# Kernel tuning notes

Hardware: AMD Instinct MI355X
Metric: run time of the kernel (lower is better)

The kernel has to match this reference:

```python
import jax, jax.numpy as jnp
import numpy as np

HIDDEN = 128
HEADS = 8
HEAD_DIM = HIDDEN // HEADS
N_NODES = 100000
N_EDGES = 1600000


def setup_inputs() -> dict:
    key = jax.random.key(0)
    ks = jax.random.split(key, 12)
    s = 1.0 / np.sqrt(HIDDEN)
    inp = {
        "x": jax.random.normal(ks[0], (N_NODES, HIDDEN), dtype=jnp.float32),
        "edge_index": jax.random.randint(ks[1], (2, N_EDGES), 0, N_NODES, dtype=jnp.int32),
        "edge_emb": jax.random.normal(ks[2], (N_EDGES, HIDDEN), dtype=jnp.float32),
        "q_w": jax.random.uniform(ks[3], (HIDDEN, HIDDEN), jnp.float32, -s, s),
        "q_b": jax.random.uniform(ks[4], (HIDDEN,), jnp.float32, -s, s),
        "k_w": jax.random.uniform(ks[5], (HIDDEN, HIDDEN), jnp.float32, -s, s),
        "k_b": jax.random.uniform(ks[6], (HIDDEN,), jnp.float32, -s, s),
        "v_w": jax.random.uniform(ks[7], (HIDDEN, HIDDEN), jnp.float32, -s, s),
        "v_b": jax.random.uniform(ks[8], (HIDDEN,), jnp.float32, -s, s),
        "out_w": jax.random.uniform(ks[9], (HIDDEN, HIDDEN), jnp.float32, -s, s),
        "out_b": jax.random.uniform(ks[10], (HIDDEN,), jnp.float32, -s, s),
        "eb_w": jax.random.uniform(ks[11], (HEADS, HIDDEN), jnp.float32, -s, s),
        "eb_b": jnp.zeros((HEADS,), dtype=jnp.float32),
    }
    return inp


def reference(x, edge_index, edge_emb, q_w, q_b, k_w, k_b, v_w, v_b, out_w, out_b, eb_w, eb_b):
    n = x.shape[0]
    # node projections -> [N, H, D]
    q = (x @ q_w.T + q_b).reshape(n, HEADS, HEAD_DIM)
    k = (x @ k_w.T + k_b).reshape(n, HEADS, HEAD_DIM)
    v = (x @ v_w.T + v_b).reshape(n, HEADS, HEAD_DIM)

    row, col = edge_index[0], edge_index[1]
    # per-edge scores: [E, H]
    scores = jnp.einsum('ehd,ehd->eh', q[row], k[col]) / jnp.sqrt(jnp.float32(HEAD_DIM))
    scores = scores + edge_emb @ eb_w.T + eb_b

    # segmented softmax over incoming edges of each destination node `row`
    seg_max = jax.ops.segment_max(scores, row, num_segments=n)  # [N, H]
    exp_scores = jnp.exp(scores - seg_max[row])
    seg_sum = jax.ops.segment_sum(exp_scores, row, num_segments=n)  # [N, H]
    attn = exp_scores / (seg_sum[row] + 1e-10)  # [E, H]

    # weighted scatter-aggregation of values
    weighted_v = attn[..., None] * v[col]  # [E, H, D]
    out = jax.ops.segment_sum(weighted_v, row, num_segments=n)  # [N, H, D]
    out = out.reshape(n, HIDDEN)
    return out @ out_w.T + out_b
```

## Files before the change

kernel.cpp:

```cpp
#include <hip/hip_runtime.h>

#define HID 128
#define NH 8

typedef __attribute__((ext_vector_type(8))) short short8;
typedef __attribute__((ext_vector_type(4))) float f32x4;

__device__ __forceinline__ unsigned short f2bf(float f) {
    unsigned int u = __float_as_uint(f);
    u = (u + 0x7FFF + ((u >> 16) & 1)) >> 16;
    return (unsigned short)u;
}
__device__ __forceinline__ float bf2f(unsigned short s) {
    return __uint_as_float((unsigned int)s << 16);
}
__device__ __forceinline__ unsigned int pack2bf(float lo, float hi) {
    return (unsigned int)f2bf(lo) | ((unsigned int)f2bf(hi) << 16);
}

__global__ void k_hist(const int* __restrict__ row, int E, int* __restrict__ count) {
    int i = blockIdx.x * blockDim.x + threadIdx.x;
    int stride = gridDim.x * blockDim.x;
    for (; i < E; i += stride) atomicAdd(&count[row[i]], 1);
}

__global__ void k_scan1(const int* __restrict__ in, int total,
                        int* __restrict__ out, int* __restrict__ bsums) {
    __shared__ int sd[256];
    int t = threadIdx.x;
    int base = blockIdx.x * 1024 + t * 4;
    int v0 = (base + 0 < total) ? in[base + 0] : 0;
    int v1 = (base + 1 < total) ? in[base + 1] : 0;
    int v2 = (base + 2 < total) ? in[base + 2] : 0;
    int v3 = (base + 3 < total) ? in[base + 3] : 0;
    int s = v0 + v1 + v2 + v3;
    sd[t] = s; __syncthreads();
    for (int off = 1; off < 256; off <<= 1) {
        int xx = (t >= off) ? sd[t - off] : 0;
        __syncthreads();
        sd[t] += xx;
        __syncthreads();
    }
    int excl = sd[t] - s;
    if (t == 255) bsums[blockIdx.x] = sd[255];
    int run = excl;
    if (base + 0 < total) out[base + 0] = run; run += v0;
    if (base + 1 < total) out[base + 1] = run; run += v1;
    if (base + 2 < total) out[base + 2] = run; run += v2;
    if (base + 3 < total) out[base + 3] = run;
}

__global__ void k_scan2(int* __restrict__ bs, int nb) {
    __shared__ int sd[128];
    int t = threadIdx.x;
    int vv = (t < nb) ? bs[t] : 0;
    sd[t] = vv; __syncthreads();
    for (int off = 1; off < 128; off <<= 1) {
        int xx = (t >= off) ? sd[t - off] : 0;
        __syncthreads();
        sd[t] += xx;
        __syncthreads();
    }
    if (t < nb) bs[t] = sd[t] - vv;
}

__global__ void k_scan3(int* __restrict__ out, int total, const int* __restrict__ bs) {
    int add = bs[blockIdx.x];
    int base = blockIdx.x * 1024 + threadIdx.x * 4;
    #pragma unroll
    for (int i = 0; i < 4; ++i)
        if (base + i < total) out[base + i] += add;
}

__global__ void k_cvtw(const float* __restrict__ qw, const float* __restrict__ kw,
                       const float* __restrict__ vw, const float* __restrict__ ow,
                       unsigned short* __restrict__ wbf) {
    int i = blockIdx.x * 256 + threadIdx.x;
    int idx = i * 4;
    int m = idx >> 14;
    int off = idx & 16383;
    const float* src = (m == 0) ? qw : (m == 1) ? kw : (m == 2) ? vw : ow;
    float4 v = *(const float4*)(src + off);
    ushort4 o;
    o.x = f2bf(v.x); o.y = f2bf(v.y); o.z = f2bf(v.z); o.w = f2bf(v.w);
    *(ushort4*)(wbf + idx) = o;
}

__global__ __launch_bounds__(256) void k_fat(
    const float* __restrict__ x, const unsigned short* __restrict__ wbf,
    const float* __restrict__ qb_, const float* __restrict__ kb_, const float* __restrict__ vb_,
    unsigned short* __restrict__ qkvbf, int n, int qblocks,
    const int* __restrict__ row, const int* __restrict__ col,
    const float* __restrict__ emb, const float* __restrict__ ebw,
    const float* __restrict__ ebb, const int* __restrict__ start,
    int* __restrict__ cursor, char* __restrict__ recs, int E)
{
    __shared__ __align__(16) char sm[17408];
    int bid = blockIdx.x;
    int t = threadIdx.x;

    if (bid < qblocks) {
        unsigned short (*xs)[136] = (unsigned short (*)[136])sm;
        int m0 = bid * 64;
        #pragma unroll
        for (int p = 0; p < 2; ++p) {
            int f = p * 256 + t;
            int r = f >> 3;
            int c16 = (f & 7) * 16;
            int node = m0 + r;
            float4 u0 = {0,0,0,0}, u1 = {0,0,0,0}, u2 = {0,0,0,0}, u3 = {0,0,0,0};
            if (node < n) {
                const float4* px = (const float4*)(x + (size_t)node * HID + c16);
                u0 = px[0]; u1 = px[1]; u2 = px[2]; u3 = px[3];
            }
            union { unsigned short u[8]; short8 v; } a, b;
            a.u[0]=f2bf(u0.x); a.u[1]=f2bf(u0.y); a.u[2]=f2bf(u0.z); a.u[3]=f2bf(u0.w);
            a.u[4]=f2bf(u1.x); a.u[5]=f2bf(u1.y); a.u[6]=f2bf(u1.z); a.u[7]=f2bf(u1.w);
            b.u[0]=f2bf(u2.x); b.u[1]=f2bf(u2.y); b.u[2]=f2bf(u2.z); b.u[3]=f2bf(u2.w);
            b.u[4]=f2bf(u3.x); b.u[5]=f2bf(u3.y); b.u[6]=f2bf(u3.z); b.u[7]=f2bf(u3.w);
            *(short8*)&xs[r][c16]     = a.v;
            *(short8*)&xs[r][c16 + 8] = b.v;
        }
        __syncthreads();

        int w = t >> 6, l = t & 63;
        int lr = l & 15, lc = l >> 4;
        short8 afr[4];
        #pragma unroll
        for (int c = 0; c < 4; ++c)
            afr[c] = *(const short8*)&xs[w * 16 + lr][c * 32 + lc * 8];

        #pragma unroll
        for (int m = 0; m < 3; ++m) {
            const float* bias = (m == 0) ? qb_ : (m == 1) ? kb_ : vb_;
            #pragma unroll
            for (int ct = 0; ct < 8; ++ct) {
                int colg = ct * 16 + lr;
                f32x4 acc = {0.f, 0.f, 0.f, 0.f};
                const unsigned short* wrow = wbf + (size_t)m * 16384 + (size_t)colg * 128 + lc * 8;
                #pragma unroll
                for (int c = 0; c < 4; ++c) {
                    short8 bfr = *(const short8*)(wrow + c * 32);
                    acc = __builtin_amdgcn_mfma_f32_16x16x32_bf16(afr[c], bfr, acc, 0, 0, 0);
                }
                float bv = bias[colg];
                #pragma unroll
                for (int r = 0; r < 4; ++r) {
                    int node = m0 + w * 16 + lc * 4 + r;
                    if (node < n)
                        qkvbf[(size_t)node * 384 + m * 128 + colg] = f2bf(acc[r] + bv);
                }
            }
        }
    } else {
        float (*Wx)[4][8][4] = (float (*)[4][8][4])sm;
        for (int i = t; i < 1024; i += 256) {
            int j = i & 3, g = (i >> 2) & 7, c = (i >> 5) & 3, h = i >> 7;
            Wx[h][c][g][j] = ebw[h * 128 + g * 16 + c * 4 + j];
        }
        float bbr[8];
        #pragma unroll
        for (int i = 0; i < 8; ++i) bbr[i] = ebb[i];
        __syncthreads();

        int l = t & 63;
        int g = l & 7;
        int sub = l >> 3;
        int e = (bid - qblocks) * 32 + (t >> 6) * 8 + sub;
        bool act = e < E;

        float p[8] = {0.f,0.f,0.f,0.f,0.f,0.f,0.f,0.f};
        if (act) {
            const float4* pe = (const float4*)(emb + (size_t)e * HID + g * 16);
            #pragma unroll
            for (int c = 0; c < 4; ++c) {
                float4 ev = pe[c];
                #pragma unroll
                for (int h = 0; h < 8; ++h) {
                    float4 wv = *(const float4*)&Wx[h][c][g][0];
                    p[h] += ev.x*wv.x + ev.y*wv.y + ev.z*wv.z + ev.w*wv.w;
                }
            }
        }
        #pragma unroll
        for (int off = 1; off < 8; off <<= 1) {
            #pragma unroll
            for (int h = 0; h < 8; ++h) p[h] += __shfl_xor(p[h], off);
        }
        if (act && g == 0) {
            int r = row[e];
            int ps = start[r] + atomicAdd(&cursor[r], 1);
            char* rp = recs + (size_t)ps * 32;
            uint4 r0;
            r0.x = (unsigned int)col[e];
            r0.y = pack2bf(p[0] + bbr[0], p[1] + bbr[1]);
            r0.z = pack2bf(p[2] + bbr[2], p[3] + bbr[3]);
            r0.w = pack2bf(p[4] + bbr[4], p[5] + bbr[5]);
            uint2 r1;
            r1.x = pack2bf(p[6] + bbr[6], p[7] + bbr[7]);
            r1.y = 0;
            *(uint4*)rp = r0;
            *(uint2*)(rp + 16) = r1;
        }
    }
}

__global__ __launch_bounds__(256) void k_attn(
    const unsigned short* __restrict__ qkvbf, const char* __restrict__ recs,
    const int* __restrict__ start, unsigned short* __restrict__ aout, int n)
{
    int node = blockIdx.x * 4 + (threadIdx.x >> 6);
    if (node >= n) return;
    int l = threadIdx.x & 63;
    int slot = l >> 3;
    int h = l & 7;
    int s0 = start[node];
    int deg = start[node + 1] - s0;

    float qf[16];
    {
        const unsigned short* qp = qkvbf + (size_t)node * 384 + h * 16;
        short8 q0 = *(const short8*)qp;
        short8 q1 = *(const short8*)(qp + 8);
        #pragma unroll
        for (int i = 0; i < 8; ++i) {
            qf[i] = bf2f((unsigned short)q0[i]);
            qf[8 + i] = bf2f((unsigned short)q1[i]);
        }
    }

    float acc[16];
    #pragma unroll
    for (int i = 0; i < 16; ++i) acc[i] = 0.f;
    float denom = 0.f;

    for (int base = 0; base < deg; base += 8) {
        int idx = base + slot;
        bool act = idx < deg;
        const char* rp = recs + (size_t)(s0 + (act ? idx : 0)) * 32;
        int c = act ? *(const int*)rp : 0;
        float eb = act ? bf2f(*(const unsigned short*)(rp + 4 + 2 * h)) : 0.f;
        const unsigned short* kv = qkvbf + (size_t)c * 384 + 128 + h * 16;
        short8 ka  = *(const short8*)kv;
        short8 kbv = *(const short8*)(kv + 8);
        short8 va  = *(const short8*)(kv + 128);
        short8 vb  = *(const short8*)(kv + 136);
        float part = 0.f;
        #pragma unroll
        for (int i = 0; i < 8; ++i) part += qf[i] * bf2f((unsigned short)ka[i]);
        #pragma unroll
        for (int i = 0; i < 8; ++i) part += qf[8 + i] * bf2f((unsigned short)kbv[i]);
        float es = act ? __expf(part * 0.25f + eb) : 0.f;
        denom += es;
        #pragma unroll
        for (int i = 0; i < 8; ++i) acc[i]     += es * bf2f((unsigned short)va[i]);
        #pragma unroll
        for (int i = 0; i < 8; ++i) acc[8 + i] += es * bf2f((unsigned short)vb[i]);
    }

    #pragma unroll
    for (int off = 8; off < 64; off <<= 1) {
        denom += __shfl_xor(denom, off);
        #pragma unroll
        for (int i = 0; i < 16; ++i) acc[i] += __shfl_xor(acc[i], off);
    }
    if (slot == 0) {
        float inv = 1.f / (denom + 1e-10f);
        uint4 o0, o1;
        o0.x = pack2bf(acc[0]*inv,  acc[1]*inv);
        o0.y = pack2bf(acc[2]*inv,  acc[3]*inv);
        o0.z = pack2bf(acc[4]*inv,  acc[5]*inv);
        o0.w = pack2bf(acc[6]*inv,  acc[7]*inv);
        o1.x = pack2bf(acc[8]*inv,  acc[9]*inv);
        o1.y = pack2bf(acc[10]*inv, acc[11]*inv);
        o1.z = pack2bf(acc[12]*inv, acc[13]*inv);
        o1.w = pack2bf(acc[14]*inv, acc[15]*inv);
        unsigned short* op = aout + (size_t)node * HID + h * 16;
        *(uint4*)op       = o0;
        *(uint4*)(op + 8) = o1;
    }
}

__global__ __launch_bounds__(256) void k_outproj_mfma(
    const unsigned short* __restrict__ aout, const unsigned short* __restrict__ wbf,
    const float* __restrict__ ob, float* __restrict__ out, int n)
{
    __shared__ unsigned short hs[64][136];
    int t = threadIdx.x;
    int m0 = blockIdx.x * 64;
    #pragma unroll
    for (int p = 0; p < 4; ++p) {
        int f = p * 256 + t;
        int r = f >> 4;
        int c8 = (f & 15) * 8;
        int node = m0 + r;
        short8 val = {0,0,0,0,0,0,0,0};
        if (node < n) val = *(const short8*)(aout + (size_t)node * HID + c8);
        *(short8*)&hs[r][c8] = val;
    }
    __syncthreads();

    int w = t >> 6, l = t & 63;
    int lr = l & 15, lc = l >> 4;
    short8 afr[4];
    #pragma unroll
    for (int c = 0; c < 4; ++c)
        afr[c] = *(const short8*)&hs[w * 16 + lr][c * 32 + lc * 8];

    #pragma unroll
    for (int ct = 0; ct < 8; ++ct) {
        int colg = ct * 16 + lr;
        f32x4 acc = {0.f, 0.f, 0.f, 0.f};
        const unsigned short* wrow = wbf + (size_t)3 * 16384 + (size_t)colg * 128 + lc * 8;
        #pragma unroll
        for (int c = 0; c < 4; ++c) {
            short8 bfr = *(const short8*)(wrow + c * 32);
            acc = __builtin_amdgcn_mfma_f32_16x16x32_bf16(afr[c], bfr, acc, 0, 0, 0);
        }
        float bv = ob[colg];
        #pragma unroll
        for (int r = 0; r < 4; ++r) {
            int node = m0 + w * 16 + lc * 4 + r;
            if (node < n)
                out[(size_t)node * HID + colg] = acc[r] + bv;
        }
    }
}

extern "C" void kernel_launch(void* const* d_in, const int* in_sizes, int n_in,
                              void* d_out, int out_size, void* d_ws, size_t ws_size,
                              hipStream_t stream) {
    const float* x   = (const float*)d_in[0];
    const int*   eix = (const int*)  d_in[1];
    const float* emb = (const float*)d_in[2];
    const float* qw  = (const float*)d_in[3];
    const float* qb  = (const float*)d_in[4];
    const float* kw  = (const float*)d_in[5];
    const float* kb  = (const float*)d_in[6];
    const float* vw  = (const float*)d_in[7];
    const float* vb  = (const float*)d_in[8];
    const float* ow  = (const float*)d_in[9];
    const float* ob  = (const float*)d_in[10];
    const float* ebw = (const float*)d_in[11];
    const float* ebb = (const float*)d_in[12];

    int n = in_sizes[0] / HID;
    int E = in_sizes[2] / HID;
    const int* row = eix;
    const int* col = eix + E;

    char* wsp = (char*)d_ws;
    auto alloc = [&](size_t bytes) -> void* {
        void* p = (void*)wsp;
        wsp += (bytes + 255) & ~(size_t)255;
        return p;
    };
    unsigned short* qkvbf = (unsigned short*)alloc((size_t)n * 384 * 2);
    unsigned short* wbf   = (unsigned short*)alloc((size_t)4 * 16384 * 2);
    char* recs            = (char*)alloc((size_t)E * 32);
    unsigned short* aout  = (unsigned short*)alloc((size_t)n * HID * 2);
    int* count            = (int*)alloc((size_t)(n + 2) * 4);
    int* startp           = (int*)alloc((size_t)(n + 2) * 4);
    int* bsums            = (int*)alloc(256 * 4);
    int* cursor           = (int*)alloc((size_t)n * 4);

    hipMemsetAsync(count, 0, (size_t)(n + 1) * sizeof(int), stream);
    hipMemsetAsync(cursor, 0, (size_t)n * sizeof(int), stream);

    k_cvtw<<<64, 256, 0, stream>>>(qw, kw, vw, ow, wbf);
    k_hist<<<2048, 256, 0, stream>>>(row, E, count);

    int total = n + 1;
    int nb = (total + 1023) / 1024;
    k_scan1<<<nb, 256, 0, stream>>>(count, total, startp, bsums);
    k_scan2<<<1, 128, 0, stream>>>(bsums, nb);
    k_scan3<<<nb, 256, 0, stream>>>(startp, total, bsums);

    int qblocks = (n + 63) / 64;
    int eblocks = (E + 31) / 32;
    k_fat<<<qblocks + eblocks, 256, 0, stream>>>(
        x, wbf, qb, kb, vb, qkvbf, n, qblocks,
        row, col, emb, ebw, ebb, startp, cursor, recs, E);

    k_attn<<<(n + 3) / 4, 256, 0, stream>>>(qkvbf, recs, startp, aout, n);
    k_outproj_mfma<<<(n + 63) / 64, 256, 0, stream>>>(aout, wbf, ob, (float*)d_out, n);
}
```

Before: 564.3 us.

## Fuse attention aggregation into output projection kernel via shared memory

Merges the per-node attention kernel with the MFMA output projection so that each 64-node block computes the aggregated head outputs, stores them in LDS, and then applies the projection directly. This removes the bf16 intermediate buffer round-trip through global memory and one kernel launch. In exchange, each wave now processes 16 nodes one after another, so a block runs longer and is more exposed to degree imbalance, and the grid has 16x fewer blocks, which lowers latency hiding for the gather-heavy loop. The hist and weight-convert launches are also swapped in order.

```diff
diff --git a/kernel.cpp b/kernel.cpp
--- a/kernel.cpp
+++ b/kernel.cpp
@@ -205,102 +205,95 @@
     }
 }
 
-__global__ __launch_bounds__(256) void k_attn(
+__global__ __launch_bounds__(256) void k_attn_outproj(
     const unsigned short* __restrict__ qkvbf, const char* __restrict__ recs,
-    const int* __restrict__ start, unsigned short* __restrict__ aout, int n)
-{
-    int node = blockIdx.x * 4 + (threadIdx.x >> 6);
-    if (node >= n) return;
-    int l = threadIdx.x & 63;
-    int slot = l >> 3;
-    int h = l & 7;
-    int s0 = start[node];
-    int deg = start[node + 1] - s0;
-
-    float qf[16];
-    {
-        const unsigned short* qp = qkvbf + (size_t)node * 384 + h * 16;
-        short8 q0 = *(const short8*)qp;
-        short8 q1 = *(const short8*)(qp + 8);
-        #pragma unroll
-        for (int i = 0; i < 8; ++i) {
-            qf[i] = bf2f((unsigned short)q0[i]);
-            qf[8 + i] = bf2f((unsigned short)q1[i]);
-        }
-    }
-
-    float acc[16];
-    #pragma unroll
-    for (int i = 0; i < 16; ++i) acc[i] = 0.f;
-    float denom = 0.f;
-
-    for (int base = 0; base < deg; base += 8) {
-        int idx = base + slot;
-        bool act = idx < deg;
-        const char* rp = recs + (size_t)(s0 + (act ? idx : 0)) * 32;
-        int c = act ? *(const int*)rp : 0;
-        float eb = act ? bf2f(*(const unsigned short*)(rp + 4 + 2 * h)) : 0.f;
-        const unsigned short* kv = qkvbf + (size_t)c * 384 + 128 + h * 16;
-        short8 ka  = *(const short8*)kv;
-        short8 kbv = *(const short8*)(kv + 8);
-        short8 va  = *(const short8*)(kv + 128);
-        short8 vb  = *(const short8*)(kv + 136);
-        float part = 0.f;
-        #pragma unroll
-        for (int i = 0; i < 8; ++i) part += qf[i] * bf2f((unsigned short)ka[i]);
-        #pragma unroll
-        for (int i = 0; i < 8; ++i) part += qf[8 + i] * bf2f((unsigned short)kbv[i]);
-        float es = act ? __expf(part * 0.25f + eb) : 0.f;
-        denom += es;
-        #pragma unroll
-        for (int i = 0; i < 8; ++i) acc[i]     += es * bf2f((unsigned short)va[i]);
-        #pragma unroll
-        for (int i = 0; i < 8; ++i) acc[8 + i] += es * bf2f((unsigned short)vb[i]);
-    }
-
-    #pragma unroll
-    for (int off = 8; off < 64; off <<= 1) {
-        denom += __shfl_xor(denom, off);
-        #pragma unroll
-        for (int i = 0; i < 16; ++i) acc[i] += __shfl_xor(acc[i], off);
-    }
-    if (slot == 0) {
-        float inv = 1.f / (denom + 1e-10f);
-        uint4 o0, o1;
-        o0.x = pack2bf(acc[0]*inv,  acc[1]*inv);
-        o0.y = pack2bf(acc[2]*inv,  acc[3]*inv);
-        o0.z = pack2bf(acc[4]*inv,  acc[5]*inv);
-        o0.w = pack2bf(acc[6]*inv,  acc[7]*inv);
-        o1.x = pack2bf(acc[8]*inv,  acc[9]*inv);
-        o1.y = pack2bf(acc[10]*inv, acc[11]*inv);
-        o1.z = pack2bf(acc[12]*inv, acc[13]*inv);
-        o1.w = pack2bf(acc[14]*inv, acc[15]*inv);
-        unsigned short* op = aout + (size_t)node * HID + h * 16;
-        *(uint4*)op       = o0;
-        *(uint4*)(op + 8) = o1;
-    }
-}
-
-__global__ __launch_bounds__(256) void k_outproj_mfma(
-    const unsigned short* __restrict__ aout, const unsigned short* __restrict__ wbf,
+    const int* __restrict__ start, const unsigned short* __restrict__ wbf,
     const float* __restrict__ ob, float* __restrict__ out, int n)
 {
     __shared__ unsigned short hs[64][136];
     int t = threadIdx.x;
     int m0 = blockIdx.x * 64;
-    #pragma unroll
-    for (int p = 0; p < 4; ++p) {
-        int f = p * 256 + t;
-        int r = f >> 4;
-        int c8 = (f & 15) * 8;
-        int node = m0 + r;
-        short8 val = {0,0,0,0,0,0,0,0};
-        if (node < n) val = *(const short8*)(aout + (size_t)node * HID + c8);
-        *(short8*)&hs[r][c8] = val;
+    int w = t >> 6, l = t & 63;
+    int slot = l >> 3;
+    int h = l & 7;
+
+    for (int ni = 0; ni < 16; ++ni) {
+        int node = m0 + w * 16 + ni;
+        if (node < n) {
+            int s0 = start[node];
+            int deg = start[node + 1] - s0;
+
+            float qf[16];
+            {
+                const unsigned short* qp = qkvbf + (size_t)node * 384 + h * 16;
+                short8 q0 = *(const short8*)qp;
+                short8 q1 = *(const short8*)(qp + 8);
+                #pragma unroll
+                for (int i = 0; i < 8; ++i) {
+                    qf[i] = bf2f((unsigned short)q0[i]);
+                    qf[8 + i] = bf2f((unsigned short)q1[i]);
+                }
+            }
+
+            float acc[16];
+            #pragma unroll
+            for (int i = 0; i < 16; ++i) acc[i] = 0.f;
+            float denom = 0.f;
+
+            for (int base = 0; base < deg; base += 8) {
+                int idx = base + slot;
+                bool act = idx < deg;
+                const char* rp = recs + (size_t)(s0 + (act ? idx : 0)) * 32;
+                int c = act ? *(const int*)rp : 0;
+                float eb = act ? bf2f(*(const unsigned short*)(rp + 4 + 2 * h)) : 0.f;
+                const unsigned short* kv = qkvbf + (size_t)c * 384 + 128 + h * 16;
+                short8 ka  = *(const short8*)kv;
+                short8 kbv = *(const short8*)(kv + 8);
+                short8 va  = *(const short8*)(kv + 128);
+                short8 vb  = *(const short8*)(kv + 136);
+                float part = 0.f;
+                #pragma unroll
+                for (int i = 0; i < 8; ++i) part += qf[i] * bf2f((unsigned short)ka[i]);
+                #pragma unroll
+                for (int i = 0; i < 8; ++i) part += qf[8 + i] * bf2f((unsigned short)kbv[i]);
+                float es = act ? __expf(part * 0.25f + eb) : 0.f;
+                denom += es;
+                #pragma unroll
+                for (int i = 0; i < 8; ++i) acc[i]     += es * bf2f((unsigned short)va[i]);
+                #pragma unroll
+                for (int i = 0; i < 8; ++i) acc[8 + i] += es * bf2f((unsigned short)vb[i]);
+            }
+
+            #pragma unroll
+            for (int off = 8; off < 64; off <<= 1) {
+                denom += __shfl_xor(denom, off);
+                #pragma unroll
+                for (int i = 0; i < 16; ++i) acc[i] += __shfl_xor(acc[i], off);
+            }
+            if (slot == 0) {
+                float inv = 1.f / (denom + 1e-10f);
+                uint4 o0, o1;
+                o0.x = pack2bf(acc[0]*inv,  acc[1]*inv);
+                o0.y = pack2bf(acc[2]*inv,  acc[3]*inv);
+                o0.z = pack2bf(acc[4]*inv,  acc[5]*inv);
+                o0.w = pack2bf(acc[6]*inv,  acc[7]*inv);
+                o1.x = pack2bf(acc[8]*inv,  acc[9]*inv);
+                o1.y = pack2bf(acc[10]*inv, acc[11]*inv);
+                o1.z = pack2bf(acc[12]*inv, acc[13]*inv);
+                o1.w = pack2bf(acc[14]*inv, acc[15]*inv);
+                unsigned short* hp = &hs[w * 16 + ni][h * 16];
+                *(uint4*)hp       = o0;
+                *(uint4*)(hp + 8) = o1;
+            }
+        } else if (slot == 0) {
+            uint4 z = {0, 0, 0, 0};
+            unsigned short* hp = &hs[w * 16 + ni][h * 16];
+            *(uint4*)hp       = z;
+            *(uint4*)(hp + 8) = z;
+        }
     }
     __syncthreads();
 
-    int w = t >> 6, l = t & 63;
     int lr = l & 15, lc = l >> 4;
     short8 afr[4];
     #pragma unroll
@@ -358,7 +351,6 @@
     unsigned short* qkvbf = (unsigned short*)alloc((size_t)n * 384 * 2);
     unsigned short* wbf   = (unsigned short*)alloc((size_t)4 * 16384 * 2);
     char* recs            = (char*)alloc((size_t)E * 32);
-    unsigned short* aout  = (unsigned short*)alloc((size_t)n * HID * 2);
     int* count            = (int*)alloc((size_t)(n + 2) * 4);
     int* startp           = (int*)alloc((size_t)(n + 2) * 4);
     int* bsums            = (int*)alloc(256 * 4);
@@ -367,8 +359,8 @@
     hipMemsetAsync(count, 0, (size_t)(n + 1) * sizeof(int), stream);
     hipMemsetAsync(cursor, 0, (size_t)n * sizeof(int), stream);
 
+    k_hist<<<2048, 256, 0, stream>>>(row, E, count);
     k_cvtw<<<64, 256, 0, stream>>>(qw, kw, vw, ow, wbf);
-    k_hist<<<2048, 256, 0, stream>>>(row, E, count);
 
     int total = n + 1;
     int nb = (total + 1023) / 1024;
@@ -382,6 +374,6 @@
         x, wbf, qb, kb, vb, qkvbf, n, qblocks,
         row, col, emb, ebw, ebb, startp, cursor, recs, E);
 
-    k_attn<<<(n + 3) / 4, 256, 0, stream>>>(qkvbf, recs, startp, aout, n);
-    k_outproj_mfma<<<(n + 63) / 64, 256, 0, stream>>>(aout, wbf, ob, (float*)d_out, n);
-}
+    k_attn_outproj<<<(n + 63) / 64, 256, 0, stream>>>(
+        qkvbf, recs, startp, wbf, ob, (float*)d_out, n);
+}
```

After: 597.7 us. +5.9%, slower.

## Store keys in FP8, split edge records into SoA, fuse init kernels

Applied to the files above, without the earlier changes.

Adds a pass that converts K from bf16 to fp8 (e4m3) per node, so the attention gather reads 16 bytes of K per head instead of 32. The 32-byte AoS edge record becomes two arrays: sorted column indices and 8 bf16 biases (16 bytes), which removes the padding bytes from record traffic. The weight-conversion and histogram kernels are merged into one launch. The risks are lower score precision from fp8 keys and an extra kernel launch plus pass over K.

```diff
diff --git a/kernel.cpp b/kernel.cpp
--- a/kernel.cpp
+++ b/kernel.cpp
@@ -5,6 +5,7 @@
 
 typedef __attribute__((ext_vector_type(8))) short short8;
 typedef __attribute__((ext_vector_type(4))) float f32x4;
+typedef __attribute__((ext_vector_type(2))) float f32x2;
 
 __device__ __forceinline__ unsigned short f2bf(float f) {
     unsigned int u = __float_as_uint(f);
@@ -18,10 +19,27 @@
     return (unsigned int)f2bf(lo) | ((unsigned int)f2bf(hi) << 16);
 }
 
-__global__ void k_hist(const int* __restrict__ row, int E, int* __restrict__ count) {
-    int i = blockIdx.x * blockDim.x + threadIdx.x;
-    int stride = gridDim.x * blockDim.x;
-    for (; i < E; i += stride) atomicAdd(&count[row[i]], 1);
+__global__ void k_init(const float* __restrict__ qw, const float* __restrict__ kw,
+                       const float* __restrict__ vw, const float* __restrict__ ow,
+                       unsigned short* __restrict__ wbf,
+                       const int* __restrict__ row, int E, int* __restrict__ count) {
+    int bid = blockIdx.x;
+    int t = threadIdx.x;
+    if (bid < 64) {
+        int i = bid * 256 + t;
+        int idx = i * 4;
+        int m = idx >> 14;
+        int off = idx & 16383;
+        const float* src = (m == 0) ? qw : (m == 1) ? kw : (m == 2) ? vw : ow;
+        float4 v = *(const float4*)(src + off);
+        ushort4 o;
+        o.x = f2bf(v.x); o.y = f2bf(v.y); o.z = f2bf(v.z); o.w = f2bf(v.w);
+        *(ushort4*)(wbf + idx) = o;
+    } else {
+        int i = (bid - 64) * 256 + t;
+        int stride = (gridDim.x - 64) * 256;
+        for (; i < E; i += stride) atomicAdd(&count[row[i]], 1);
+    }
 }
 
 __global__ void k_scan1(const int* __restrict__ in, int total,
@@ -72,20 +90,6 @@
         if (base + i < total) out[base + i] += add;
 }
 
-__global__ void k_cvtw(const float* __restrict__ qw, const float* __restrict__ kw,
-                       const float* __restrict__ vw, const float* __restrict__ ow,
-                       unsigned short* __restrict__ wbf) {
-    int i = blockIdx.x * 256 + threadIdx.x;
-    int idx = i * 4;
-    int m = idx >> 14;
-    int off = idx & 16383;
-    const float* src = (m == 0) ? qw : (m == 1) ? kw : (m == 2) ? vw : ow;
-    float4 v = *(const float4*)(src + off);
-    ushort4 o;
-    o.x = f2bf(v.x); o.y = f2bf(v.y); o.z = f2bf(v.z); o.w = f2bf(v.w);
-    *(ushort4*)(wbf + idx) = o;
-}
-
 __global__ __launch_bounds__(256) void k_fat(
     const float* __restrict__ x, const unsigned short* __restrict__ wbf,
     const float* __restrict__ qb_, const float* __restrict__ kb_, const float* __restrict__ vb_,
@@ -93,7 +97,8 @@
     const int* __restrict__ row, const int* __restrict__ col,
     const float* __restrict__ emb, const float* __restrict__ ebw,
     const float* __restrict__ ebb, const int* __restrict__ start,
-    int* __restrict__ cursor, char* __restrict__ recs, int E)
+    int* __restrict__ cursor, int* __restrict__ col_sorted,
+    unsigned short* __restrict__ bias_s, int E)
 {
     __shared__ __align__(16) char sm[17408];
     int bid = blockIdx.x;
@@ -190,23 +195,40 @@
         if (act && g == 0) {
             int r = row[e];
             int ps = start[r] + atomicAdd(&cursor[r], 1);
-            char* rp = recs + (size_t)ps * 32;
-            uint4 r0;
-            r0.x = (unsigned int)col[e];
-            r0.y = pack2bf(p[0] + bbr[0], p[1] + bbr[1]);
-            r0.z = pack2bf(p[2] + bbr[2], p[3] + bbr[3]);
-            r0.w = pack2bf(p[4] + bbr[4], p[5] + bbr[5]);
-            uint2 r1;
-            r1.x = pack2bf(p[6] + bbr[6], p[7] + bbr[7]);
-            r1.y = 0;
-            *(uint4*)rp = r0;
-            *(uint2*)(rp + 16) = r1;
-        }
-    }
+            col_sorted[ps] = col[e];
+            uint4 bv;
+            bv.x = pack2bf(p[0] + bbr[0], p[1] + bbr[1]);
+            bv.y = pack2bf(p[2] + bbr[2], p[3] + bbr[3]);
+            bv.z = pack2bf(p[4] + bbr[4], p[5] + bbr[5]);
+            bv.w = pack2bf(p[6] + bbr[6], p[7] + bbr[7]);
+            *(uint4*)(bias_s + (size_t)ps * 8) = bv;
+        }
+    }
+}
+
+__global__ __launch_bounds__(256) void k_cvtk(
+    const unsigned short* __restrict__ qkvbf, unsigned char* __restrict__ kp8, int n)
+{
+    int i = blockIdx.x * 256 + threadIdx.x;
+    int node = i >> 4;
+    int c8 = (i & 15) * 8;
+    if (node >= n) return;
+    short8 kv = *(const short8*)(qkvbf + (size_t)node * 384 + 128 + c8);
+    float f[8];
+    #pragma unroll
+    for (int j = 0; j < 8; ++j) f[j] = bf2f((unsigned short)kv[j]);
+    unsigned int lo = 0, hi = 0;
+    lo = (unsigned int)__builtin_amdgcn_cvt_pk_fp8_f32(f[0], f[1], (int)lo, false);
+    lo = (unsigned int)__builtin_amdgcn_cvt_pk_fp8_f32(f[2], f[3], (int)lo, true);
+    hi = (unsigned int)__builtin_amdgcn_cvt_pk_fp8_f32(f[4], f[5], (int)hi, false);
+    hi = (unsigned int)__builtin_amdgcn_cvt_pk_fp8_f32(f[6], f[7], (int)hi, true);
+    uint2 o; o.x = lo; o.y = hi;
+    *(uint2*)(kp8 + (size_t)node * HID + c8) = o;
 }
 
 __global__ __launch_bounds__(256) void k_attn(
-    const unsigned short* __restrict__ qkvbf, const char* __restrict__ recs,
+    const unsigned short* __restrict__ qkvbf, const unsigned char* __restrict__ kp8,
+    const int* __restrict__ cols, const unsigned short* __restrict__ bias_s,
     const int* __restrict__ start, unsigned short* __restrict__ aout, int n)
 {
     int node = blockIdx.x * 4 + (threadIdx.x >> 6);
@@ -237,19 +259,29 @@
     for (int base = 0; base < deg; base += 8) {
         int idx = base + slot;
         bool act = idx < deg;
-        const char* rp = recs + (size_t)(s0 + (act ? idx : 0)) * 32;
-        int c = act ? *(const int*)rp : 0;
-        float eb = act ? bf2f(*(const unsigned short*)(rp + 4 + 2 * h)) : 0.f;
-        const unsigned short* kv = qkvbf + (size_t)c * 384 + 128 + h * 16;
-        short8 ka  = *(const short8*)kv;
-        short8 kbv = *(const short8*)(kv + 8);
-        short8 va  = *(const short8*)(kv + 128);
-        short8 vb  = *(const short8*)(kv + 136);
+        int sidx = s0 + (act ? idx : 0);
+        int c = act ? cols[sidx] : 0;
+        float eb = act ? bf2f(bias_s[(size_t)sidx * 8 + h]) : 0.f;
+        uint4 kw4 = *(const uint4*)(kp8 + (size_t)c * HID + h * 16);
+        const unsigned short* vp = qkvbf + (size_t)c * 384 + 256 + h * 16;
+        short8 va = *(const short8*)vp;
+        short8 vb = *(const short8*)(vp + 8);
+
         float part = 0.f;
-        #pragma unroll
-        for (int i = 0; i < 8; ++i) part += qf[i] * bf2f((unsigned short)ka[i]);
-        #pragma unroll
-        for (int i = 0; i < 8; ++i) part += qf[8 + i] * bf2f((unsigned short)kbv[i]);
+        {
+            f32x2 d0 = __builtin_amdgcn_cvt_pk_f32_fp8((int)kw4.x, false);
+            f32x2 d1 = __builtin_amdgcn_cvt_pk_f32_fp8((int)kw4.x, true);
+            f32x2 d2 = __builtin_amdgcn_cvt_pk_f32_fp8((int)kw4.y, false);
+            f32x2 d3 = __builtin_amdgcn_cvt_pk_f32_fp8((int)kw4.y, true);
+            f32x2 d4 = __builtin_amdgcn_cvt_pk_f32_fp8((int)kw4.z, false);
+            f32x2 d5 = __builtin_amdgcn_cvt_pk_f32_fp8((int)kw4.z, true);
+            f32x2 d6 = __builtin_amdgcn_cvt_pk_f32_fp8((int)kw4.w, false);
+            f32x2 d7 = __builtin_amdgcn_cvt_pk_f32_fp8((int)kw4.w, true);
+            part += qf[0]*d0[0] + qf[1]*d0[1] + qf[2]*d1[0] + qf[3]*d1[1];
+            part += qf[4]*d2[0] + qf[5]*d2[1] + qf[6]*d3[0] + qf[7]*d3[1];
+            part += qf[8]*d4[0] + qf[9]*d4[1] + qf[10]*d5[0] + qf[11]*d5[1];
+            part += qf[12]*d6[0] + qf[13]*d6[1] + qf[14]*d7[0] + qf[15]*d7[1];
+        }
         float es = act ? __expf(part * 0.25f + eb) : 0.f;
         denom += es;
         #pragma unroll
@@ -356,8 +388,10 @@
         return p;
     };
     unsigned short* qkvbf = (unsigned short*)alloc((size_t)n * 384 * 2);
+    unsigned char* kp8    = (unsigned char*)alloc((size_t)n * HID);
     unsigned short* wbf   = (unsigned short*)alloc((size_t)4 * 16384 * 2);
-    char* recs            = (char*)alloc((size_t)E * 32);
+    int* col_sorted       = (int*)alloc((size_t)E * 4);
+    unsigned short* bias_s= (unsigned short*)alloc((size_t)E * 8 * 2);
     unsigned short* aout  = (unsigned short*)alloc((size_t)n * HID * 2);
     int* count            = (int*)alloc((size_t)(n + 2) * 4);
     int* startp           = (int*)alloc((size_t)(n + 2) * 4);
@@ -367,8 +401,7 @@
     hipMemsetAsync(count, 0, (size_t)(n + 1) * sizeof(int), stream);
     hipMemsetAsync(cursor, 0, (size_t)n * sizeof(int), stream);
 
-    k_cvtw<<<64, 256, 0, stream>>>(qw, kw, vw, ow, wbf);
-    k_hist<<<2048, 256, 0, stream>>>(row, E, count);
+    k_init<<<64 + 2048, 256, 0, stream>>>(qw, kw, vw, ow, wbf, row, E, count);
 
     int total = n + 1;
     int nb = (total + 1023) / 1024;
@@ -380,8 +413,11 @@
     int eblocks = (E + 31) / 32;
     k_fat<<<qblocks + eblocks, 256, 0, stream>>>(
         x, wbf, qb, kb, vb, qkvbf, n, qblocks,
-        row, col, emb, ebw, ebb, startp, cursor, recs, E);
-
-    k_attn<<<(n + 3) / 4, 256, 0, stream>>>(qkvbf, recs, startp, aout, n);
+        row, col, emb, ebw, ebb, startp, cursor, col_sorted, bias_s, E);
+
+    k_cvtk<<<(n * 16 + 255) / 256, 256, 0, stream>>>(qkvbf, kp8, n);
+
+    k_attn<<<(n + 3) / 4, 256, 0, stream>>>(qkvbf, kp8, col_sorted, bias_s,
+                                            startp, aout, n);
     k_outproj_mfma<<<(n + 63) / 64, 256, 0, stream>>>(aout, wbf, ob, (float*)d_out, n);
 }
```

Measured after the change: 557.2 us. About the same (-1.3%).
